# Kernel tuning notes

Hardware: AMD Instinct MI355X
Metric: run time of the kernel (lower is better)

Reference implementation:

```python
import jax, jax.numpy as jnp
import numpy as np
import math

E = 8          # num_experts (= max_expert_num)
M = 1024       # hidden_size
H = 4096       # expert FFN dim (4*hidden)
B, S = 4, 4096 # batch, seq
CAP_FACTOR = 1.0
MIN_CAPACITY = 4


def setup_inputs() -> dict:
    key = jax.random.key(0)
    ks = jax.random.split(key, 5)
    hidden_states = jax.random.normal(ks[0], (B, S, M), dtype=jnp.float32)
    wg = jax.random.normal(ks[1], (M, E), dtype=jnp.float32) * (M ** -0.5)  # gate Linear (no bias, as in TopKGate)
    w1 = jax.random.normal(ks[2], (E, M, H), dtype=jnp.float32) * (M ** -0.5)
    b1 = jnp.zeros((E, H), dtype=jnp.float32)
    w2 = jax.random.normal(ks[3], (E, H, M), dtype=jnp.float32) * (H ** -0.5)
    b2 = jnp.zeros((E, M), dtype=jnp.float32)
    return {"hidden_states": hidden_states, "wg": wg, "w1": w1, "b1": b1, "w2": w2, "b2": b2}


def reference(hidden_states, wg, w1, b1, w2, b2):
    b, s_len, m = hidden_states.shape
    x = hidden_states.reshape(-1, m)            # [s, m], s = tokens
    s = x.shape[0]
    capacity = max(int(math.ceil(s / E * CAP_FACTOR)), MIN_CAPACITY)  # static

    # ---- top-1 gating (DeepSpeed top1gating, fp32, no jitter, no RTS) ----
    logits = x.astype(jnp.float32) @ wg          # [s, e]
    gates = jax.nn.softmax(logits, axis=1)
    idx = jnp.argmax(gates, axis=1)              # chosen expert per token
    mask1 = jax.nn.one_hot(idx, E, dtype=jnp.float32)
    exp_counts = jnp.sum(mask1, axis=0).astype(jnp.int32)
    ce = jnp.mean(mask1, axis=0)                 # fraction routed per expert (pre-drop)
    me = jnp.mean(gates, axis=0)
    l_aux = jnp.sum(me * ce) * E                 # load-balancing loss

    # position of each token within its expert's queue; drop past capacity
    locations = jnp.cumsum(mask1, axis=0) - 1.0  # [s, e]
    loc = jnp.sum(locations * mask1, axis=1).astype(jnp.int32)  # [s]
    keep = (loc < capacity).astype(jnp.float32)  # capacity drop mask
    gate_s = jnp.sum(gates * mask1, axis=1) * keep
    loc_c = jnp.clip(loc, 0, capacity - 1)

    # ---- dispatch: scatter tokens to [E, C, M] slots (equiv. to einsum('sec,sm->ecm')) ----
    dispatched = jnp.zeros((E, capacity, m), dtype=x.dtype).at[idx, loc_c].add(x * keep[:, None])

    # ---- grouped expert GEMMs (MLP with GELU) ----
    h = jax.nn.gelu(jnp.einsum('ecm,emh->ech', dispatched, w1) + b1[:, None, :])
    eout = jnp.einsum('ech,ehm->ecm', h, w2) + b2[:, None, :]

    # ---- combine: gather back and scale by gate value (dropped tokens -> 0) ----
    out = eout[idx, loc_c] * gate_s[:, None]     # [s, m]
    return out.reshape(b, s_len, m), l_aux, exp_counts
```

## Files before the change

### kernel.cpp

```cpp
#include <hip/hip_runtime.h>
#include <hip/hip_bf16.h>

#define TOKENS 16384
#define MDIM   1024
#define HDIM   4096
#define NEXP   8
#define EGRP   4
#define CAP    2048
#define NKT1   (MDIM / 64)
#define NKT2   (HDIM / 64)

typedef __attribute__((ext_vector_type(8))) short bf16x8;
typedef __attribute__((ext_vector_type(4))) float f32x4;

__device__ __forceinline__ short f2bf(float x) {
  unsigned u = __float_as_uint(x);
  unsigned r = (u + 0x7fffu + ((u >> 16) & 1u)) >> 16;
  return (short)r;
}

__device__ __forceinline__ unsigned bfbits(float x) {
  unsigned u = __float_as_uint(x);
  return u + 0x7fffu + ((u >> 16) & 1u);
}

__device__ __forceinline__ float gelu_f(float x) {
  float u = 1.5957691216057308f * (x + 0.044715f * x * x * x);
  float e = __expf(u);
  return x * (1.f - 1.f / (e + 1.f));
}

__global__ __launch_bounds__(256) void gating_kernel(
    const float* __restrict__ x, const float* __restrict__ wg,
    int* __restrict__ idx, float* __restrict__ gate,
    float* __restrict__ mepart, short* __restrict__ xb) {
  __shared__ float me_s[NEXP];
  int tid = threadIdx.x, wid = tid >> 6, lane = tid & 63;
  if (tid < NEXP) me_s[tid] = 0.f;
  __syncthreads();
  int t = blockIdx.x * 4 + wid;
  float acc[NEXP];
#pragma unroll
  for (int e = 0; e < NEXP; e++) acc[e] = 0.f;
  const float4* xr = (const float4*)(x + (size_t)t * MDIM);
  short* xbr = xb + (size_t)t * MDIM + lane * 16;
#pragma unroll
  for (int j = 0; j < 4; j++) {
    float4 xv = xr[lane * 4 + j];
    short4 bv; bv.x = f2bf(xv.x); bv.y = f2bf(xv.y); bv.z = f2bf(xv.z); bv.w = f2bf(xv.w);
    ((short4*)(xbr))[j] = bv;
    int base = lane * 16 + j * 4;
    const float* xp = &xv.x;
#pragma unroll
    for (int i = 0; i < 4; i++) {
      float xi = xp[i];
      const float4* wr = (const float4*)(wg + (size_t)(base + i) * NEXP);
      float4 w0 = wr[0], w1 = wr[1];
      acc[0] += xi * w0.x; acc[1] += xi * w0.y; acc[2] += xi * w0.z; acc[3] += xi * w0.w;
      acc[4] += xi * w1.x; acc[5] += xi * w1.y; acc[6] += xi * w1.z; acc[7] += xi * w1.w;
    }
  }
#pragma unroll
  for (int off = 32; off > 0; off >>= 1)
#pragma unroll
    for (int e = 0; e < NEXP; e++) acc[e] += __shfl_xor(acc[e], off, 64);
  if (lane == 0) {
    float mx = acc[0]; int ai = 0;
#pragma unroll
    for (int e = 1; e < NEXP; e++) if (acc[e] > mx) { mx = acc[e]; ai = e; }
    float ex[NEXP]; float se = 0.f;
#pragma unroll
    for (int e = 0; e < NEXP; e++) { ex[e] = __expf(acc[e] - mx); se += ex[e]; }
    float inv = 1.f / se;
#pragma unroll
    for (int e = 0; e < NEXP; e++) atomicAdd(&me_s[e], ex[e] * inv);
    idx[t] = ai;
    gate[t] = inv;
  }
  __syncthreads();
  if (tid < NEXP) mepart[blockIdx.x * NEXP + tid] = me_s[tid];
}

__global__ __launch_bounds__(1024) void scan_kernel(
    const int* __restrict__ idx, float* __restrict__ gate,
    int* __restrict__ s2t, int* __restrict__ counts,
    const float* __restrict__ mepart, float* __restrict__ out_tail) {
  __shared__ int wcnt[16][NEXP];
  __shared__ int wbase[16][NEXP];
  __shared__ int totc[NEXP];
  __shared__ float red2[1024];
  int tid = threadIdx.x, wid = tid >> 6, lane = tid & 63;
  unsigned long long ltmask = (1ull << lane) - 1ull;
  int myexp[16], myloc[16];
  int cnt[NEXP];
#pragma unroll
  for (int e = 0; e < NEXP; e++) cnt[e] = 0;
  int base_tok = wid * 1024;
#pragma unroll
  for (int p = 0; p < 16; p++) {
    int e = idx[base_tok + p * 64 + lane];
    myexp[p] = e;
    int pos = 0;
#pragma unroll
    for (int e2 = 0; e2 < NEXP; e2++) {
      unsigned long long b = __ballot(e == e2);
      if (e == e2) pos = cnt[e2] + __popcll(b & ltmask);
      cnt[e2] += __popcll(b);
    }
    myloc[p] = pos;
  }
  if (lane < NEXP) wcnt[wid][lane] = cnt[lane];
  __syncthreads();
  if (tid < 128) {
    int w = tid >> 3, e = tid & 7;
    int s = 0;
    for (int w2 = 0; w2 < w; w2++) s += wcnt[w2][e];
    wbase[w][e] = s;
  }
  __syncthreads();
#pragma unroll
  for (int p = 0; p < 16; p++) {
    int i = base_tok + p * 64 + lane;
    int e = myexp[p];
    int loc = wbase[wid][e] + myloc[p];
    if (loc < CAP) s2t[e * CAP + loc] = i;
    else           gate[i] = 0.f;
  }
  if (tid < NEXP) {
    int tot = 0;
#pragma unroll
    for (int w = 0; w < 16; w++) tot += wcnt[w][tid];
    counts[tid] = tot;
    totc[tid] = tot;
  }
  float s = 0.f;
  int e2 = tid & 7;
  for (int r = tid >> 3; r < (TOKENS / 4); r += 128) s += mepart[(size_t)r * NEXP + e2];
  red2[tid] = s;
  __syncthreads();
#pragma unroll
  for (int off = 512; off >= 8; off >>= 1) {
    if (tid < off) red2[tid] += red2[tid + off];
    __syncthreads();
  }
  if (tid == 0) {
    float la = 0.f;
    for (int k = 0; k < NEXP; k++)
      la += (red2[k] / (float)TOKENS) * ((float)totc[k] / (float)TOKENS);
    out_tail[0] = la * (float)NEXP;
  }
  if (tid < NEXP) out_tail[1 + tid] = (float)totc[tid];
}

__global__ __launch_bounds__(256) void transpose_cvt_kernel(
    const float* __restrict__ in, short* __restrict__ out, int R, int Cc) {
  __shared__ short tile[64][72];
  int e = blockIdx.z;
  const float* in_e = in + (size_t)e * R * Cc;
  short* out_e = out + (size_t)e * R * Cc;
  int r0 = blockIdx.y * 64, c0 = blockIdx.x * 64;
  int tid = threadIdx.x;
#pragma unroll
  for (int i = 0; i < 4; i++) {
    int linear = tid + 256 * i;
    int r = linear >> 4;
    int f4 = linear & 15;
    float4 v = *(const float4*)(in_e + (size_t)(r0 + r) * Cc + c0 + f4 * 4);
    int c = f4 * 4;
    tile[c + 0][r] = f2bf(v.x);
    tile[c + 1][r] = f2bf(v.y);
    tile[c + 2][r] = f2bf(v.z);
    tile[c + 3][r] = f2bf(v.w);
  }
  __syncthreads();
#pragma unroll
  for (int i = 0; i < 4; i++) {
    int linear = tid + 256 * i;
    int c = linear >> 4;
    int s4 = linear & 15;
    short4 s;
    s.x = tile[c][s4 * 4 + 0]; s.y = tile[c][s4 * 4 + 1];
    s.z = tile[c][s4 * 4 + 2]; s.w = tile[c][s4 * 4 + 3];
    *(short4*)(out_e + (size_t)(c0 + c) * R + r0 + s4 * 4) = s;
  }
}

__device__ __forceinline__ void bar() {
  asm volatile("" ::: "memory");
  __builtin_amdgcn_s_barrier();
  asm volatile("" ::: "memory");
}
__device__ __forceinline__ void lgkm0() {
  asm volatile("s_waitcnt lgkmcnt(0)" ::: "memory");
  __builtin_amdgcn_sched_barrier(0);
}
__device__ __forceinline__ void vm_bar8() {
  asm volatile("s_waitcnt vmcnt(8)" ::: "memory");
  __builtin_amdgcn_s_barrier();
  asm volatile("" ::: "memory");
}
__device__ __forceinline__ void vm_bar6() {
  asm volatile("s_waitcnt vmcnt(6)" ::: "memory");
  __builtin_amdgcn_s_barrier();
  asm volatile("" ::: "memory");
}
__device__ __forceinline__ void vm_bar0() {
  asm volatile("s_waitcnt vmcnt(0)" ::: "memory");
  __builtin_amdgcn_s_barrier();
  asm volatile("" ::: "memory");
}

#define GLL(gp, lp) __builtin_amdgcn_global_load_lds(                                   \
    (const __attribute__((address_space(1))) void*)(gp),                                \
    (__attribute__((address_space(3))) void*)(lp), 16, 0, 0)

__global__ __launch_bounds__(512, 2) void gemm1_kernel(
    const short* __restrict__ xb, const int* __restrict__ s2t,
    const short* __restrict__ W1t, const float* __restrict__ b1,
    short* __restrict__ Hh, const short* __restrict__ zrow, int eg) {
  __shared__ __align__(16) short ldsA[2][256 * 64];
  __shared__ __align__(16) short ldsB[2][256 * 64];
  int bz = blockIdx.z, bm = blockIdx.y, bn = blockIdx.x;
  int e_abs = eg + bz;
  int tid = threadIdx.x, lane = tid & 63, w = tid >> 6;
  int v = tid >> 3;
  int sl = tid & 7;

  const short* aptr[4];
#pragma unroll
  for (int q = 0; q < 4; q++) {
    int r = q * 64 + v;
    int tok = s2t[e_abs * CAP + bm * 256 + r];
    const short* basep = (tok >= 0) ? (xb + (size_t)tok * MDIM) : zrow;
    aptr[q] = basep + ((sl ^ (r & 7)) * 8);
  }
  const short* Be = W1t + ((size_t)e_abs * HDIM + (size_t)bn * 256) * MDIM;
  const short* bptr[2][2];
#pragma unroll
  for (int h = 0; h < 2; h++)
#pragma unroll
    for (int j = 0; j < 2; j++) {
      int r = j * 128 + (v >> 5) * 64 + (v & 31) + h * 32;
      bptr[h][j] = Be + (size_t)r * MDIM + ((sl ^ (r & 7)) * 8);
    }
  asm volatile("" ::: "memory");

  int ldsa_base[4], ldsb_base[2][2];
#pragma unroll
  for (int q = 0; q < 4; q++) ldsa_base[q] = (q * 64 + w * 8) * 64;
#pragma unroll
  for (int h = 0; h < 2; h++)
#pragma unroll
    for (int j = 0; j < 2; j++)
      ldsb_base[h][j] = (j * 128 + h * 32 + (w >> 2) * 64 + (w & 3) * 8) * 64;

  GLL(aptr[0] + 0,        &ldsA[0][ldsa_base[0]]);
  GLL(aptr[2] + 0,        &ldsA[0][ldsa_base[2]]);
  GLL(bptr[0][0] + 0,     &ldsB[0][ldsb_base[0][0]]);
  GLL(bptr[0][1] + 0,     &ldsB[0][ldsb_base[0][1]]);
  GLL(bptr[1][0] + 0,     &ldsB[0][ldsb_base[1][0]]);
  GLL(bptr[1][1] + 0,     &ldsB[0][ldsb_base[1][1]]);
  GLL(aptr[1] + 0,        &ldsA[0][ldsa_base[1]]);
  GLL(aptr[3] + 0,        &ldsA[0][ldsa_base[3]]);
  GLL(aptr[0] + 64,       &ldsA[1][ldsa_base[0]]);
  GLL(aptr[2] + 64,       &ldsA[1][ldsa_base[2]]);
  GLL(bptr[0][0] + 64,    &ldsB[1][ldsb_base[0][0]]);
  GLL(bptr[0][1] + 64,    &ldsB[1][ldsb_base[0][1]]);
  GLL(bptr[1][0] + 64,    &ldsB[1][ldsb_base[1][0]]);
  GLL(bptr[1][1] + 64,    &ldsB[1][ldsb_base[1][1]]);
  GLL(aptr[1] + 64,       &ldsA[1][ldsa_base[1]]);
  GLL(aptr[3] + 64,       &ldsA[1][ldsa_base[3]]);
  vm_bar8();

  int wm = w >> 2, wn = w & 3;
  int ln = lane & 15, q4 = lane >> 4;
  int offk0 = ((q4 ^ (lane & 7)) * 8);
  int offk1 = (((4 + q4) ^ (lane & 7)) * 8);
  int arowbase = wm * 128 + ln;
  int browbase = wn * 64 + ln;

  f32x4 acc[8][4];
  f32x4 zero = {0.f, 0.f, 0.f, 0.f};
#pragma unroll
  for (int a = 0; a < 8; a++)
#pragma unroll
    for (int b = 0; b < 4; b++) acc[a][b] = zero;

  for (int t = 0; t < NKT1; ++t) {
    int cur = t & 1;
    const short* La = ldsA[cur];
    const short* Lb = ldsB[cur];
    int kts = (t + 2) * 64;
    bool st = (t + 2) < NKT1;
    bool steady = t < (NKT1 - 2);
    bf16x8 af[4][2], bf0[2][2], bf1[2][2];
#pragma unroll
    for (int rt = 0; rt < 4; rt++) {
      int ro = (arowbase + rt * 16) * 64;
      af[rt][0] = *(const bf16x8*)(La + ro + offk0);
      af[rt][1] = *(const bf16x8*)(La + ro + offk1);
    }
#pragma unroll
    for (int c = 0; c < 2; c++) {
      int ro = (browbase + c * 16) * 64;
      bf0[c][0] = *(const bf16x8*)(Lb + ro + offk0);
      bf0[c][1] = *(const bf16x8*)(Lb + ro + offk1);
    }
    bar();
    lgkm0();
    __builtin_amdgcn_s_setprio(1);
#pragma unroll
    for (int kk = 0; kk < 2; kk++)
#pragma unroll
      for (int rt = 0; rt < 4; rt++)
#pragma unroll
        for (int c = 0; c < 2; c++)
          acc[rt][c] = __builtin_amdgcn_mfma_f32_16x16x32_bf16(bf0[c][kk], af[rt][kk], acc[rt][c], 0, 0, 0);
    __builtin_amdgcn_s_setprio(0);
    bar();
    if (st) {
      GLL(aptr[0] + kts,    &ldsA[cur][ldsa_base[0]]);
      GLL(aptr[2] + kts,    &ldsA[cur][ldsa_base[2]]);
      GLL(bptr[0][0] + kts, &ldsB[cur][ldsb_base[0][0]]);
      GLL(bptr[0][1] + kts, &ldsB[cur][ldsb_base[0][1]]);
    }
#pragma unroll
    for (int c = 0; c < 2; c++) {
      int ro = (browbase + (c + 2) * 16) * 64;
      bf1[c][0] = *(const bf16x8*)(Lb + ro + offk0);
      bf1[c][1] = *(const bf16x8*)(Lb + ro + offk1);
    }
    bar();
    lgkm0();
    __builtin_amdgcn_s_setprio(1);
#pragma unroll
    for (int kk = 0; kk < 2; kk++)
#pragma unroll
      for (int rt = 0; rt < 4; rt++)
#pragma unroll
        for (int c = 0; c < 2; c++)
          acc[rt][c + 2] = __builtin_amdgcn_mfma_f32_16x16x32_bf16(bf1[c][kk], af[rt][kk], acc[rt][c + 2], 0, 0, 0);
    __builtin_amdgcn_s_setprio(0);
    bar();
    if (st) {
      GLL(bptr[1][0] + kts, &ldsB[cur][ldsb_base[1][0]]);
      GLL(bptr[1][1] + kts, &ldsB[cur][ldsb_base[1][1]]);
    }
#pragma unroll
    for (int rt = 0; rt < 4; rt++) {
      int ro = (arowbase + 64 + rt * 16) * 64;
      af[rt][0] = *(const bf16x8*)(La + ro + offk0);
      af[rt][1] = *(const bf16x8*)(La + ro + offk1);
    }
    bar();
    lgkm0();
    __builtin_amdgcn_s_setprio(1);
#pragma unroll
    for (int kk = 0; kk < 2; kk++)
#pragma unroll
      for (int rt = 0; rt < 4; rt++)
#pragma unroll
        for (int c = 0; c < 2; c++)
          acc[4 + rt][c] = __builtin_amdgcn_mfma_f32_16x16x32_bf16(bf0[c][kk], af[rt][kk], acc[4 + rt][c], 0, 0, 0);
    __builtin_amdgcn_s_setprio(0);
    bar();
    if (st) {
      GLL(aptr[1] + kts,    &ldsA[cur][ldsa_base[1]]);
      GLL(aptr[3] + kts,    &ldsA[cur][ldsa_base[3]]);
    }
    bar();
    lgkm0();
    __builtin_amdgcn_s_setprio(1);
#pragma unroll
    for (int kk = 0; kk < 2; kk++)
#pragma unroll
      for (int rt = 0; rt < 4; rt++)
#pragma unroll
        for (int c = 0; c < 2; c++)
          acc[4 + rt][c + 2] = __builtin_amdgcn_mfma_f32_16x16x32_bf16(bf1[c][kk], af[rt][kk], acc[4 + rt][c + 2], 0, 0, 0);
    __builtin_amdgcn_s_setprio(0);
    if (steady) vm_bar8(); else vm_bar0();
  }

#pragma unroll
  for (int rt = 0; rt < 8; rt++) {
    int caprow = bm * 256 + wm * 128 + rt * 16 + ln;
    size_t rowoff = ((size_t)bz * CAP + caprow) * HDIM;
#pragma unroll
    for (int c = 0; c < 4; c++) {
      int colb = bn * 256 + wn * 64 + c * 16 + q4 * 4;
      float4 bias = *(const float4*)(b1 + (size_t)e_abs * HDIM + colb);
      unsigned u0 = bfbits(gelu_f(acc[rt][c][0] + bias.x));
      unsigned u1 = bfbits(gelu_f(acc[rt][c][1] + bias.y));
      unsigned u2 = bfbits(gelu_f(acc[rt][c][2] + bias.z));
      unsigned u3 = bfbits(gelu_f(acc[rt][c][3] + bias.w));
      uint2 pk;
      pk.x = __builtin_amdgcn_perm(u1, u0, 0x07060302u);
      pk.y = __builtin_amdgcn_perm(u3, u2, 0x07060302u);
      *(uint2*)(Hh + rowoff + colb) = pk;
    }
  }
}

__global__ __launch_bounds__(512, 2) void gemm2_kernel(
    const short* __restrict__ Hh, const short* __restrict__ W2t,
    const float* __restrict__ b2, const int* __restrict__ s2t,
    const float* __restrict__ gate, float* __restrict__ out, int eg) {
  __shared__ __align__(16) short ldsA[2][128 * 64];
  __shared__ __align__(16) short ldsB[2][256 * 64];
  int bz = blockIdx.z, bm = blockIdx.y, bn = blockIdx.x;
  int e_abs = eg + bz;
  int tid = threadIdx.x, lane = tid & 63, w = tid >> 6;
  int v = tid >> 3, sl = tid & 7;
  const short* Ae = Hh + ((size_t)bz * CAP + (size_t)bm * 128) * HDIM;
  const short* Be = W2t + ((size_t)e_abs * MDIM + (size_t)bn * 256) * HDIM;
  const short* aptr[2];
#pragma unroll
  for (int h = 0; h < 2; h++) {
    int r = (v >> 5) * 64 + (v & 31) + h * 32;
    aptr[h] = Ae + (size_t)r * HDIM + ((sl ^ (r & 7)) * 8);
  }
  const short* bptr[4];
#pragma unroll
  for (int q = 0; q < 4; q++) {
    int r = q * 64 + v;
    bptr[q] = Be + (size_t)r * HDIM + ((sl ^ (r & 7)) * 8);
  }
  int ldsa_base[2], ldsb_base[4];
#pragma unroll
  for (int h = 0; h < 2; h++) ldsa_base[h] = (h * 32 + (w >> 2) * 64 + (w & 3) * 8) * 64;
#pragma unroll
  for (int q = 0; q < 4; q++) ldsb_base[q] = (q * 64 + w * 8) * 64;

  GLL(aptr[0] + 0,  &ldsA[0][ldsa_base[0]]);
  GLL(bptr[0] + 0,  &ldsB[0][ldsb_base[0]]);
  GLL(bptr[1] + 0,  &ldsB[0][ldsb_base[1]]);
  GLL(bptr[2] + 0,  &ldsB[0][ldsb_base[2]]);
  GLL(bptr[3] + 0,  &ldsB[0][ldsb_base[3]]);
  GLL(aptr[1] + 0,  &ldsA[0][ldsa_base[1]]);
  GLL(aptr[0] + 64, &ldsA[1][ldsa_base[0]]);
  GLL(bptr[0] + 64, &ldsB[1][ldsb_base[0]]);
  GLL(bptr[1] + 64, &ldsB[1][ldsb_base[1]]);
  GLL(bptr[2] + 64, &ldsB[1][ldsb_base[2]]);
  GLL(bptr[3] + 64, &ldsB[1][ldsb_base[3]]);
  asm volatile("s_waitcnt vmcnt(5)" ::: "memory");
  __builtin_amdgcn_s_barrier();
  asm volatile("" ::: "memory");

  int wm = w >> 2, wn = w & 3;
  int ln = lane & 15, q4 = lane >> 4;
  int offk0 = ((q4 ^ (lane & 7)) * 8);
  int offk1 = (((4 + q4) ^ (lane & 7)) * 8);
  int arowbase = wm * 64 + ln;
  int browbase = wn * 64 + ln;

  f32x4 acc[4][4];
  f32x4 zero = {0.f, 0.f, 0.f, 0.f};
#pragma unroll
  for (int a = 0; a < 4; a++)
#pragma unroll
    for (int b = 0; b < 4; b++) acc[a][b] = zero;

  for (int t = 0; t < NKT2; ++t) {
    int cur = t & 1;
    const short* La = ldsA[cur];
    const short* Lb = ldsB[cur];
    bool steady = t < (NKT2 - 2);
    bf16x8 af[2][2], bf[4][2];
    if (t + 1 < NKT2) { GLL(aptr[1] + (t + 1) * 64, &ldsA[cur ^ 1][ldsa_base[1]]); }
#pragma unroll
    for (int rt = 0; rt < 2; rt++) {
      int ro = (arowbase + rt * 16) * 64;
      af[rt][0] = *(const bf16x8*)(La + ro + offk0);
      af[rt][1] = *(const bf16x8*)(La + ro + offk1);
    }
#pragma unroll
    for (int c = 0; c < 4; c++) {
      int ro = (browbase + c * 16) * 64;
      bf[c][0] = *(const bf16x8*)(Lb + ro + offk0);
      bf[c][1] = *(const bf16x8*)(Lb + ro + offk1);
    }
    bar();
    lgkm0();
    __builtin_amdgcn_s_setprio(1);
#pragma unroll
    for (int kk = 0; kk < 2; kk++)
#pragma unroll
      for (int rt = 0; rt < 2; rt++)
#pragma unroll
        for (int c = 0; c < 4; c++)
          acc[rt][c] = __builtin_amdgcn_mfma_f32_16x16x32_bf16(bf[c][kk], af[rt][kk], acc[rt][c], 0, 0, 0);
    __builtin_amdgcn_s_setprio(0);
    if (steady) vm_bar6(); else vm_bar0();
    if (t + 2 < NKT2) {
      int kts = (t + 2) * 64;
      GLL(aptr[0] + kts, &ldsA[cur][ldsa_base[0]]);
      GLL(bptr[0] + kts, &ldsB[cur][ldsb_base[0]]);
      GLL(bptr[1] + kts, &ldsB[cur][ldsb_base[1]]);
      GLL(bptr[2] + kts, &ldsB[cur][ldsb_base[2]]);
      GLL(bptr[3] + kts, &ldsB[cur][ldsb_base[3]]);
    }
#pragma unroll
    for (int rt = 0; rt < 2; rt++) {
      int ro = (arowbase + 32 + rt * 16) * 64;
      af[rt][0] = *(const bf16x8*)(La + ro + offk0);
      af[rt][1] = *(const bf16x8*)(La + ro + offk1);
    }
    bar();
    lgkm0();
    __builtin_amdgcn_s_setprio(1);
#pragma unroll
    for (int kk = 0; kk < 2; kk++)
#pragma unroll
      for (int rt = 0; rt < 2; rt++)
#pragma unroll
        for (int c = 0; c < 4; c++)
          acc[2 + rt][c] = __builtin_amdgcn_mfma_f32_16x16x32_bf16(bf[c][kk], af[rt][kk], acc[2 + rt][c], 0, 0, 0);
    __builtin_amdgcn_s_setprio(0);
    if (steady) vm_bar6(); else vm_bar0();
  }

#pragma unroll
  for (int rt = 0; rt < 4; rt++) {
    int caprow = bm * 128 + wm * 64 + rt * 16 + ln;
    int token = s2t[e_abs * CAP + caprow];
    if (token < 0) continue;
    float g = gate[token];
    float* orow = out + (size_t)token * MDIM;
#pragma unroll
    for (int c = 0; c < 4; c++) {
      int colb = bn * 256 + wn * 64 + c * 16 + q4 * 4;
      float4 bias = *(const float4*)(b2 + (size_t)e_abs * MDIM + colb);
      float4 vv;
      vv.x = (acc[rt][c][0] + bias.x) * g;
      vv.y = (acc[rt][c][1] + bias.y) * g;
      vv.z = (acc[rt][c][2] + bias.z) * g;
      vv.w = (acc[rt][c][3] + bias.w) * g;
      *(float4*)(orow + colb) = vv;
    }
  }
}

__global__ __launch_bounds__(256) void zerodrop_kernel(
    const float* __restrict__ gate, float* __restrict__ out) {
  int t = blockIdx.x;
  if (gate[t] != 0.f) return;
  float4 z = {0.f, 0.f, 0.f, 0.f};
  ((float4*)(out + (size_t)t * MDIM))[threadIdx.x] = z;
}

extern "C" void kernel_launch(void* const* d_in, const int* in_sizes, int n_in,
                              void* d_out, int out_size, void* d_ws, size_t ws_size,
                              hipStream_t stream) {
  const float* x  = (const float*)d_in[0];
  const float* wg = (const float*)d_in[1];
  const float* w1 = (const float*)d_in[2];
  const float* b1 = (const float*)d_in[3];
  const float* w2 = (const float*)d_in[4];
  const float* b2 = (const float*)d_in[5];
  float* out = (float*)d_out;

  char* ws = (char*)d_ws;
  size_t off = 0;
  auto alloc = [&](size_t n) { char* ptr = ws + off; off += (n + 255) & ~(size_t)255; return ptr; };
  short* W1t  = (short*)alloc((size_t)NEXP * MDIM * HDIM * 2);
  short* W2t  = (short*)alloc((size_t)NEXP * MDIM * HDIM * 2);
  short* Hh   = (short*)alloc((size_t)EGRP * CAP * HDIM * 2);
  short* xb   = (short*)alloc((size_t)TOKENS * MDIM * 2);
  short* zrow = (short*)alloc((size_t)MDIM * 2);
  int*   idx  = (int*)  alloc(TOKENS * 4);
  float* gate = (float*)alloc(TOKENS * 4);
  int*   s2t  = (int*)  alloc(NEXP * CAP * 4);
  float* mep  = (float*)alloc((TOKENS / 4) * NEXP * 4);
  int*   cnts = (int*)  alloc(NEXP * 4);
  if (ws_size < off) return;

  hipMemsetAsync(s2t, 0xFF, NEXP * CAP * 4, stream);
  hipMemsetAsync(zrow, 0, MDIM * 2, stream);

  gating_kernel<<<TOKENS / 4, 256, 0, stream>>>(x, wg, idx, gate, mep, xb);
  scan_kernel<<<1, 1024, 0, stream>>>(idx, gate, s2t, cnts, mep, out + (size_t)TOKENS * MDIM);
  transpose_cvt_kernel<<<dim3(HDIM / 64, MDIM / 64, NEXP), 256, 0, stream>>>(w1, W1t, MDIM, HDIM);
  transpose_cvt_kernel<<<dim3(MDIM / 64, HDIM / 64, NEXP), 256, 0, stream>>>(w2, W2t, HDIM, MDIM);
  for (int g = 0; g < 2; g++) {
    gemm1_kernel<<<dim3(HDIM / 256, CAP / 256, EGRP), 512, 0, stream>>>(xb, s2t, W1t, b1, Hh, zrow, g * EGRP);
    gemm2_kernel<<<dim3(MDIM / 256, CAP / 128, EGRP), 512, 0, stream>>>(Hh, W2t, b2, s2t, gate, out, g * EGRP);
  }
  zerodrop_kernel<<<TOKENS, 256, 0, stream>>>(gate, out);
}
```

Baseline: 933.3 us.

## Restructure expert GEMM pipelines with fewer barriers, triple-buffered B, and block swizzle

Both expert GEMM kernels are reworked. Their K-loops drop the intermediate barrier/lgkm waits and issue all MFMAs for a fragment set back to back. gemm1 loads B rows contiguously and prefetches half of A one stage ahead. gemm2 triple-buffers the B tile in LDS and loads the full A tile per step. A flat-index swizzle remaps block IDs so consecutive blocks cover different M/N tiles, aiming at better cache locality. The changes cut synchronisation overhead and improve load/compute overlap, at the cost of more LDS in gemm2 and possible occupancy loss or LDS race hazards from the removed barriers.

```diff
diff --git a/kernel.cpp b/kernel.cpp
--- a/kernel.cpp
+++ b/kernel.cpp
@@ -185,22 +185,13 @@
   }
 }
 
-__device__ __forceinline__ void bar() {
-  asm volatile("" ::: "memory");
-  __builtin_amdgcn_s_barrier();
-  asm volatile("" ::: "memory");
-}
-__device__ __forceinline__ void lgkm0() {
-  asm volatile("s_waitcnt lgkmcnt(0)" ::: "memory");
-  __builtin_amdgcn_sched_barrier(0);
-}
 __device__ __forceinline__ void vm_bar8() {
   asm volatile("s_waitcnt vmcnt(8)" ::: "memory");
   __builtin_amdgcn_s_barrier();
   asm volatile("" ::: "memory");
 }
-__device__ __forceinline__ void vm_bar6() {
-  asm volatile("s_waitcnt vmcnt(6)" ::: "memory");
+__device__ __forceinline__ void vm_bar4() {
+  asm volatile("s_waitcnt vmcnt(4)" ::: "memory");
   __builtin_amdgcn_s_barrier();
   asm volatile("" ::: "memory");
 }
@@ -220,7 +211,9 @@
     short* __restrict__ Hh, const short* __restrict__ zrow, int eg) {
   __shared__ __align__(16) short ldsA[2][256 * 64];
   __shared__ __align__(16) short ldsB[2][256 * 64];
-  int bz = blockIdx.z, bm = blockIdx.y, bn = blockIdx.x;
+  int flat = blockIdx.x + 16 * blockIdx.y + 128 * blockIdx.z;
+  int swz = (flat & 7) * 64 + (flat >> 3);
+  int bn = swz & 15, bm = (swz >> 4) & 7, bz = swz >> 7;
   int e_abs = eg + bz;
   int tid = threadIdx.x, lane = tid & 63, w = tid >> 6;
   int v = tid >> 3;
@@ -235,41 +228,32 @@
     aptr[q] = basep + ((sl ^ (r & 7)) * 8);
   }
   const short* Be = W1t + ((size_t)e_abs * HDIM + (size_t)bn * 256) * MDIM;
-  const short* bptr[2][2];
-#pragma unroll
-  for (int h = 0; h < 2; h++)
-#pragma unroll
-    for (int j = 0; j < 2; j++) {
-      int r = j * 128 + (v >> 5) * 64 + (v & 31) + h * 32;
-      bptr[h][j] = Be + (size_t)r * MDIM + ((sl ^ (r & 7)) * 8);
-    }
+  const short* bptr[4];
+#pragma unroll
+  for (int q = 0; q < 4; q++) {
+    int r = q * 64 + v;
+    bptr[q] = Be + (size_t)r * MDIM + ((sl ^ (r & 7)) * 8);
+  }
   asm volatile("" ::: "memory");
 
-  int ldsa_base[4], ldsb_base[2][2];
-#pragma unroll
-  for (int q = 0; q < 4; q++) ldsa_base[q] = (q * 64 + w * 8) * 64;
-#pragma unroll
-  for (int h = 0; h < 2; h++)
-#pragma unroll
-    for (int j = 0; j < 2; j++)
-      ldsb_base[h][j] = (j * 128 + h * 32 + (w >> 2) * 64 + (w & 3) * 8) * 64;
-
-  GLL(aptr[0] + 0,        &ldsA[0][ldsa_base[0]]);
-  GLL(aptr[2] + 0,        &ldsA[0][ldsa_base[2]]);
-  GLL(bptr[0][0] + 0,     &ldsB[0][ldsb_base[0][0]]);
-  GLL(bptr[0][1] + 0,     &ldsB[0][ldsb_base[0][1]]);
-  GLL(bptr[1][0] + 0,     &ldsB[0][ldsb_base[1][0]]);
-  GLL(bptr[1][1] + 0,     &ldsB[0][ldsb_base[1][1]]);
-  GLL(aptr[1] + 0,        &ldsA[0][ldsa_base[1]]);
-  GLL(aptr[3] + 0,        &ldsA[0][ldsa_base[3]]);
-  GLL(aptr[0] + 64,       &ldsA[1][ldsa_base[0]]);
-  GLL(aptr[2] + 64,       &ldsA[1][ldsa_base[2]]);
-  GLL(bptr[0][0] + 64,    &ldsB[1][ldsb_base[0][0]]);
-  GLL(bptr[0][1] + 64,    &ldsB[1][ldsb_base[0][1]]);
-  GLL(bptr[1][0] + 64,    &ldsB[1][ldsb_base[1][0]]);
-  GLL(bptr[1][1] + 64,    &ldsB[1][ldsb_base[1][1]]);
-  GLL(aptr[1] + 64,       &ldsA[1][ldsa_base[1]]);
-  GLL(aptr[3] + 64,       &ldsA[1][ldsa_base[3]]);
+  int ldsa_base[4], ldsb_base[4];
+#pragma unroll
+  for (int q = 0; q < 4; q++) { ldsa_base[q] = (q * 64 + w * 8) * 64; ldsb_base[q] = (q * 64 + w * 8) * 64; }
+
+  GLL(aptr[0] + 0,  &ldsA[0][ldsa_base[0]]);
+  GLL(aptr[2] + 0,  &ldsA[0][ldsa_base[2]]);
+  GLL(bptr[0] + 0,  &ldsB[0][ldsb_base[0]]);
+  GLL(bptr[1] + 0,  &ldsB[0][ldsb_base[1]]);
+  GLL(bptr[2] + 0,  &ldsB[0][ldsb_base[2]]);
+  GLL(bptr[3] + 0,  &ldsB[0][ldsb_base[3]]);
+  GLL(aptr[1] + 0,  &ldsA[0][ldsa_base[1]]);
+  GLL(aptr[3] + 0,  &ldsA[0][ldsa_base[3]]);
+  GLL(aptr[0] + 64, &ldsA[1][ldsa_base[0]]);
+  GLL(aptr[2] + 64, &ldsA[1][ldsa_base[2]]);
+  GLL(bptr[0] + 64, &ldsB[1][ldsb_base[0]]);
+  GLL(bptr[1] + 64, &ldsB[1][ldsb_base[1]]);
+  GLL(bptr[2] + 64, &ldsB[1][ldsb_base[2]]);
+  GLL(bptr[3] + 64, &ldsB[1][ldsb_base[3]]);
   vm_bar8();
 
   int wm = w >> 2, wn = w & 3;
@@ -290,10 +274,13 @@
     int cur = t & 1;
     const short* La = ldsA[cur];
     const short* Lb = ldsB[cur];
-    int kts = (t + 2) * 64;
-    bool st = (t + 2) < NKT1;
     bool steady = t < (NKT1 - 2);
-    bf16x8 af[4][2], bf0[2][2], bf1[2][2];
+    bf16x8 af[4][2], bfr[4][2];
+    if (t + 1 < NKT1) {
+      int k1 = (t + 1) * 64;
+      GLL(aptr[1] + k1, &ldsA[cur ^ 1][ldsa_base[1]]);
+      GLL(aptr[3] + k1, &ldsA[cur ^ 1][ldsa_base[3]]);
+    }
 #pragma unroll
     for (int rt = 0; rt < 4; rt++) {
       int ro = (arowbase + rt * 16) * 64;
@@ -301,50 +288,29 @@
       af[rt][1] = *(const bf16x8*)(La + ro + offk1);
     }
 #pragma unroll
-    for (int c = 0; c < 2; c++) {
+    for (int c = 0; c < 4; c++) {
       int ro = (browbase + c * 16) * 64;
-      bf0[c][0] = *(const bf16x8*)(Lb + ro + offk0);
-      bf0[c][1] = *(const bf16x8*)(Lb + ro + offk1);
-    }
-    bar();
-    lgkm0();
+      bfr[c][0] = *(const bf16x8*)(Lb + ro + offk0);
+      bfr[c][1] = *(const bf16x8*)(Lb + ro + offk1);
+    }
     __builtin_amdgcn_s_setprio(1);
 #pragma unroll
-    for (int kk = 0; kk < 2; kk++)
-#pragma unroll
-      for (int rt = 0; rt < 4; rt++)
-#pragma unroll
-        for (int c = 0; c < 2; c++)
-          acc[rt][c] = __builtin_amdgcn_mfma_f32_16x16x32_bf16(bf0[c][kk], af[rt][kk], acc[rt][c], 0, 0, 0);
+    for (int rt = 0; rt < 4; rt++)
+#pragma unroll
+      for (int c = 0; c < 4; c++) {
+        acc[rt][c] = __builtin_amdgcn_mfma_f32_16x16x32_bf16(bfr[c][0], af[rt][0], acc[rt][c], 0, 0, 0);
+        acc[rt][c] = __builtin_amdgcn_mfma_f32_16x16x32_bf16(bfr[c][1], af[rt][1], acc[rt][c], 0, 0, 0);
+      }
     __builtin_amdgcn_s_setprio(0);
-    bar();
-    if (st) {
-      GLL(aptr[0] + kts,    &ldsA[cur][ldsa_base[0]]);
-      GLL(aptr[2] + kts,    &ldsA[cur][ldsa_base[2]]);
-      GLL(bptr[0][0] + kts, &ldsB[cur][ldsb_base[0][0]]);
-      GLL(bptr[0][1] + kts, &ldsB[cur][ldsb_base[0][1]]);
-    }
-#pragma unroll
-    for (int c = 0; c < 2; c++) {
-      int ro = (browbase + (c + 2) * 16) * 64;
-      bf1[c][0] = *(const bf16x8*)(Lb + ro + offk0);
-      bf1[c][1] = *(const bf16x8*)(Lb + ro + offk1);
-    }
-    bar();
-    lgkm0();
-    __builtin_amdgcn_s_setprio(1);
-#pragma unroll
-    for (int kk = 0; kk < 2; kk++)
-#pragma unroll
-      for (int rt = 0; rt < 4; rt++)
-#pragma unroll
-        for (int c = 0; c < 2; c++)
-          acc[rt][c + 2] = __builtin_amdgcn_mfma_f32_16x16x32_bf16(bf1[c][kk], af[rt][kk], acc[rt][c + 2], 0, 0, 0);
-    __builtin_amdgcn_s_setprio(0);
-    bar();
-    if (st) {
-      GLL(bptr[1][0] + kts, &ldsB[cur][ldsb_base[1][0]]);
-      GLL(bptr[1][1] + kts, &ldsB[cur][ldsb_base[1][1]]);
+    if (steady) vm_bar8(); else vm_bar0();
+    if (t + 2 < NKT1) {
+      int kts = (t + 2) * 64;
+      GLL(aptr[0] + kts, &ldsA[cur][ldsa_base[0]]);
+      GLL(aptr[2] + kts, &ldsA[cur][ldsa_base[2]]);
+      GLL(bptr[0] + kts, &ldsB[cur][ldsb_base[0]]);
+      GLL(bptr[1] + kts, &ldsB[cur][ldsb_base[1]]);
+      GLL(bptr[2] + kts, &ldsB[cur][ldsb_base[2]]);
+      GLL(bptr[3] + kts, &ldsB[cur][ldsb_base[3]]);
     }
 #pragma unroll
     for (int rt = 0; rt < 4; rt++) {
@@ -352,32 +318,14 @@
       af[rt][0] = *(const bf16x8*)(La + ro + offk0);
       af[rt][1] = *(const bf16x8*)(La + ro + offk1);
     }
-    bar();
-    lgkm0();
     __builtin_amdgcn_s_setprio(1);
 #pragma unroll
-    for (int kk = 0; kk < 2; kk++)
-#pragma unroll
-      for (int rt = 0; rt < 4; rt++)
-#pragma unroll
-        for (int c = 0; c < 2; c++)
-          acc[4 + rt][c] = __builtin_amdgcn_mfma_f32_16x16x32_bf16(bf0[c][kk], af[rt][kk], acc[4 + rt][c], 0, 0, 0);
-    __builtin_amdgcn_s_setprio(0);
-    bar();
-    if (st) {
-      GLL(aptr[1] + kts,    &ldsA[cur][ldsa_base[1]]);
-      GLL(aptr[3] + kts,    &ldsA[cur][ldsa_base[3]]);
-    }
-    bar();
-    lgkm0();
-    __builtin_amdgcn_s_setprio(1);
-#pragma unroll
-    for (int kk = 0; kk < 2; kk++)
-#pragma unroll
-      for (int rt = 0; rt < 4; rt++)
-#pragma unroll
-        for (int c = 0; c < 2; c++)
-          acc[4 + rt][c + 2] = __builtin_amdgcn_mfma_f32_16x16x32_bf16(bf1[c][kk], af[rt][kk], acc[4 + rt][c + 2], 0, 0, 0);
+    for (int rt = 0; rt < 4; rt++)
+#pragma unroll
+      for (int c = 0; c < 4; c++) {
+        acc[4 + rt][c] = __builtin_amdgcn_mfma_f32_16x16x32_bf16(bfr[c][0], af[rt][0], acc[4 + rt][c], 0, 0, 0);
+        acc[4 + rt][c] = __builtin_amdgcn_mfma_f32_16x16x32_bf16(bfr[c][1], af[rt][1], acc[4 + rt][c], 0, 0, 0);
+      }
     __builtin_amdgcn_s_setprio(0);
     if (steady) vm_bar8(); else vm_bar0();
   }
@@ -407,8 +355,10 @@
     const float* __restrict__ b2, const int* __restrict__ s2t,
     const float* __restrict__ gate, float* __restrict__ out, int eg) {
   __shared__ __align__(16) short ldsA[2][128 * 64];
-  __shared__ __align__(16) short ldsB[2][256 * 64];
-  int bz = blockIdx.z, bm = blockIdx.y, bn = blockIdx.x;
+  __shared__ __align__(16) short ldsB[3][256 * 64];
+  int flat = blockIdx.x + 4 * blockIdx.y + 64 * blockIdx.z;
+  int swz = (flat & 7) * 32 + (flat >> 3);
+  int bn = swz & 3, bm = (swz >> 2) & 15, bz = swz >> 6;
   int e_abs = eg + bz;
   int tid = threadIdx.x, lane = tid & 63, w = tid >> 6;
   int v = tid >> 3, sl = tid & 7;
@@ -417,7 +367,7 @@
   const short* aptr[2];
 #pragma unroll
   for (int h = 0; h < 2; h++) {
-    int r = (v >> 5) * 64 + (v & 31) + h * 32;
+    int r = h * 64 + v;
     aptr[h] = Ae + (size_t)r * HDIM + ((sl ^ (r & 7)) * 8);
   }
   const short* bptr[4];
@@ -428,24 +378,21 @@
   }
   int ldsa_base[2], ldsb_base[4];
 #pragma unroll
-  for (int h = 0; h < 2; h++) ldsa_base[h] = (h * 32 + (w >> 2) * 64 + (w & 3) * 8) * 64;
+  for (int h = 0; h < 2; h++) ldsa_base[h] = (h * 64 + w * 8) * 64;
 #pragma unroll
   for (int q = 0; q < 4; q++) ldsb_base[q] = (q * 64 + w * 8) * 64;
 
   GLL(aptr[0] + 0,  &ldsA[0][ldsa_base[0]]);
+  GLL(aptr[1] + 0,  &ldsA[0][ldsa_base[1]]);
   GLL(bptr[0] + 0,  &ldsB[0][ldsb_base[0]]);
   GLL(bptr[1] + 0,  &ldsB[0][ldsb_base[1]]);
   GLL(bptr[2] + 0,  &ldsB[0][ldsb_base[2]]);
   GLL(bptr[3] + 0,  &ldsB[0][ldsb_base[3]]);
-  GLL(aptr[1] + 0,  &ldsA[0][ldsa_base[1]]);
-  GLL(aptr[0] + 64, &ldsA[1][ldsa_base[0]]);
   GLL(bptr[0] + 64, &ldsB[1][ldsb_base[0]]);
   GLL(bptr[1] + 64, &ldsB[1][ldsb_base[1]]);
   GLL(bptr[2] + 64, &ldsB[1][ldsb_base[2]]);
   GLL(bptr[3] + 64, &ldsB[1][ldsb_base[3]]);
-  asm volatile("s_waitcnt vmcnt(5)" ::: "memory");
-  __builtin_amdgcn_s_barrier();
-  asm volatile("" ::: "memory");
+  vm_bar4();
 
   int wm = w >> 2, wn = w & 3;
   int ln = lane & 15, q4 = lane >> 4;
@@ -461,15 +408,29 @@
 #pragma unroll
     for (int b = 0; b < 4; b++) acc[a][b] = zero;
 
+  short* b_cur = ldsB[0];
+  short* b_n1  = ldsB[1];
+  short* b_n2  = ldsB[2];
+
   for (int t = 0; t < NKT2; ++t) {
-    int cur = t & 1;
-    const short* La = ldsA[cur];
-    const short* Lb = ldsB[cur];
+    const short* La = ldsA[t & 1];
+    const short* Lb = b_cur;
     bool steady = t < (NKT2 - 2);
-    bf16x8 af[2][2], bf[4][2];
-    if (t + 1 < NKT2) { GLL(aptr[1] + (t + 1) * 64, &ldsA[cur ^ 1][ldsa_base[1]]); }
-#pragma unroll
-    for (int rt = 0; rt < 2; rt++) {
+    if (t + 1 < NKT2) {
+      int k1 = (t + 1) * 64;
+      GLL(aptr[0] + k1, &ldsA[(t + 1) & 1][ldsa_base[0]]);
+      GLL(aptr[1] + k1, &ldsA[(t + 1) & 1][ldsa_base[1]]);
+    }
+    if (t + 2 < NKT2) {
+      int k2 = (t + 2) * 64;
+      GLL(bptr[0] + k2, b_n2 + ldsb_base[0]);
+      GLL(bptr[1] + k2, b_n2 + ldsb_base[1]);
+      GLL(bptr[2] + k2, b_n2 + ldsb_base[2]);
+      GLL(bptr[3] + k2, b_n2 + ldsb_base[3]);
+    }
+    bf16x8 af[4][2], bf[4][2];
+#pragma unroll
+    for (int rt = 0; rt < 4; rt++) {
       int ro = (arowbase + rt * 16) * 64;
       af[rt][0] = *(const bf16x8*)(La + ro + offk0);
       af[rt][1] = *(const bf16x8*)(La + ro + offk1);
@@ -480,44 +441,17 @@
       bf[c][0] = *(const bf16x8*)(Lb + ro + offk0);
       bf[c][1] = *(const bf16x8*)(Lb + ro + offk1);
     }
-    bar();
-    lgkm0();
     __builtin_amdgcn_s_setprio(1);
 #pragma unroll
-    for (int kk = 0; kk < 2; kk++)
-#pragma unroll
-      for (int rt = 0; rt < 2; rt++)
-#pragma unroll
-        for (int c = 0; c < 4; c++)
-          acc[rt][c] = __builtin_amdgcn_mfma_f32_16x16x32_bf16(bf[c][kk], af[rt][kk], acc[rt][c], 0, 0, 0);
+    for (int rt = 0; rt < 4; rt++)
+#pragma unroll
+      for (int c = 0; c < 4; c++) {
+        acc[rt][c] = __builtin_amdgcn_mfma_f32_16x16x32_bf16(bf[c][0], af[rt][0], acc[rt][c], 0, 0, 0);
+        acc[rt][c] = __builtin_amdgcn_mfma_f32_16x16x32_bf16(bf[c][1], af[rt][1], acc[rt][c], 0, 0, 0);
+      }
     __builtin_amdgcn_s_setprio(0);
-    if (steady) vm_bar6(); else vm_bar0();
-    if (t + 2 < NKT2) {
-      int kts = (t + 2) * 64;
-      GLL(aptr[0] + kts, &ldsA[cur][ldsa_base[0]]);
-      GLL(bptr[0] + kts, &ldsB[cur][ldsb_base[0]]);
-      GLL(bptr[1] + kts, &ldsB[cur][ldsb_base[1]]);
-      GLL(bptr[2] + kts, &ldsB[cur][ldsb_base[2]]);
-      GLL(bptr[3] + kts, &ldsB[cur][ldsb_base[3]]);
-    }
-#pragma unroll
-    for (int rt = 0; rt < 2; rt++) {
-      int ro = (arowbase + 32 + rt * 16) * 64;
-      af[rt][0] = *(const bf16x8*)(La + ro + offk0);
-      af[rt][1] = *(const bf16x8*)(La + ro + offk1);
-    }
-    bar();
-    lgkm0();
-    __builtin_amdgcn_s_setprio(1);
-#pragma unroll
-    for (int kk = 0; kk < 2; kk++)
-#pragma unroll
-      for (int rt = 0; rt < 2; rt++)
-#pragma unroll
-        for (int c = 0; c < 4; c++)
-          acc[2 + rt][c] = __builtin_amdgcn_mfma_f32_16x16x32_bf16(bf[c][kk], af[rt][kk], acc[2 + rt][c], 0, 0, 0);
-    __builtin_amdgcn_s_setprio(0);
-    if (steady) vm_bar6(); else vm_bar0();
+    if (steady) vm_bar4(); else vm_bar0();
+    short* tmp = b_cur; b_cur = b_n1; b_n1 = b_n2; b_n2 = tmp;
   }
 
 #pragma unroll
```

New measurement: 888.3 us. 4.8% less time.

## Swizzle GEMM block order, trim gemm1 barriers, retile gemm2 to 128x128

Applied to the files above, without the earlier changes.

Both expert GEMMs now remap their flat block index so that consecutive blocks spread across the grid, aiming for better L2 reuse of weights and activations. gemm1 drops the extra barrier and lgkmcnt waits around each MFMA phase and relies on the vmcnt barriers to order LDS reuse, which should cut synchronisation stalls. gemm2 moves from 512-thread 128x256 tiles with a two-deep staged prefetch to 256-thread 128x128 tiles with a simple one-ahead double buffer and a full vmcnt(0) barrier every K step. This doubles the gemm2 grid but may expose more global-load latency.

```diff
diff --git a/kernel.cpp b/kernel.cpp
--- a/kernel.cpp
+++ b/kernel.cpp
@@ -185,22 +185,8 @@
   }
 }
 
-__device__ __forceinline__ void bar() {
-  asm volatile("" ::: "memory");
-  __builtin_amdgcn_s_barrier();
-  asm volatile("" ::: "memory");
-}
-__device__ __forceinline__ void lgkm0() {
-  asm volatile("s_waitcnt lgkmcnt(0)" ::: "memory");
-  __builtin_amdgcn_sched_barrier(0);
-}
 __device__ __forceinline__ void vm_bar8() {
   asm volatile("s_waitcnt vmcnt(8)" ::: "memory");
-  __builtin_amdgcn_s_barrier();
-  asm volatile("" ::: "memory");
-}
-__device__ __forceinline__ void vm_bar6() {
-  asm volatile("s_waitcnt vmcnt(6)" ::: "memory");
   __builtin_amdgcn_s_barrier();
   asm volatile("" ::: "memory");
 }
@@ -220,7 +206,9 @@
     short* __restrict__ Hh, const short* __restrict__ zrow, int eg) {
   __shared__ __align__(16) short ldsA[2][256 * 64];
   __shared__ __align__(16) short ldsB[2][256 * 64];
-  int bz = blockIdx.z, bm = blockIdx.y, bn = blockIdx.x;
+  int flat = blockIdx.x + 16 * blockIdx.y + 128 * blockIdx.z;
+  int swz = (flat & 7) * 64 + (flat >> 3);
+  int bn = swz & 15, bm = (swz >> 4) & 7, bz = swz >> 7;
   int e_abs = eg + bz;
   int tid = threadIdx.x, lane = tid & 63, w = tid >> 6;
   int v = tid >> 3;
@@ -295,19 +283,17 @@
     bool steady = t < (NKT1 - 2);
     bf16x8 af[4][2], bf0[2][2], bf1[2][2];
 #pragma unroll
+    for (int c = 0; c < 2; c++) {
+      int ro = (browbase + c * 16) * 64;
+      bf0[c][0] = *(const bf16x8*)(Lb + ro + offk0);
+      bf0[c][1] = *(const bf16x8*)(Lb + ro + offk1);
+    }
+#pragma unroll
     for (int rt = 0; rt < 4; rt++) {
       int ro = (arowbase + rt * 16) * 64;
       af[rt][0] = *(const bf16x8*)(La + ro + offk0);
       af[rt][1] = *(const bf16x8*)(La + ro + offk1);
     }
-#pragma unroll
-    for (int c = 0; c < 2; c++) {
-      int ro = (browbase + c * 16) * 64;
-      bf0[c][0] = *(const bf16x8*)(Lb + ro + offk0);
-      bf0[c][1] = *(const bf16x8*)(Lb + ro + offk1);
-    }
-    bar();
-    lgkm0();
     __builtin_amdgcn_s_setprio(1);
 #pragma unroll
     for (int kk = 0; kk < 2; kk++)
@@ -317,7 +303,7 @@
         for (int c = 0; c < 2; c++)
           acc[rt][c] = __builtin_amdgcn_mfma_f32_16x16x32_bf16(bf0[c][kk], af[rt][kk], acc[rt][c], 0, 0, 0);
     __builtin_amdgcn_s_setprio(0);
-    bar();
+    if (steady) vm_bar8(); else vm_bar0();
     if (st) {
       GLL(aptr[0] + kts,    &ldsA[cur][ldsa_base[0]]);
       GLL(aptr[2] + kts,    &ldsA[cur][ldsa_base[2]]);
@@ -330,8 +316,6 @@
       bf1[c][0] = *(const bf16x8*)(Lb + ro + offk0);
       bf1[c][1] = *(const bf16x8*)(Lb + ro + offk1);
     }
-    bar();
-    lgkm0();
     __builtin_amdgcn_s_setprio(1);
 #pragma unroll
     for (int kk = 0; kk < 2; kk++)
@@ -341,7 +325,7 @@
         for (int c = 0; c < 2; c++)
           acc[rt][c + 2] = __builtin_amdgcn_mfma_f32_16x16x32_bf16(bf1[c][kk], af[rt][kk], acc[rt][c + 2], 0, 0, 0);
     __builtin_amdgcn_s_setprio(0);
-    bar();
+    if (steady) vm_bar8(); else vm_bar0();
     if (st) {
       GLL(bptr[1][0] + kts, &ldsB[cur][ldsb_base[1][0]]);
       GLL(bptr[1][1] + kts, &ldsB[cur][ldsb_base[1][1]]);
@@ -352,8 +336,6 @@
       af[rt][0] = *(const bf16x8*)(La + ro + offk0);
       af[rt][1] = *(const bf16x8*)(La + ro + offk1);
     }
-    bar();
-    lgkm0();
     __builtin_amdgcn_s_setprio(1);
 #pragma unroll
     for (int kk = 0; kk < 2; kk++)
@@ -363,13 +345,11 @@
         for (int c = 0; c < 2; c++)
           acc[4 + rt][c] = __builtin_amdgcn_mfma_f32_16x16x32_bf16(bf0[c][kk], af[rt][kk], acc[4 + rt][c], 0, 0, 0);
     __builtin_amdgcn_s_setprio(0);
-    bar();
+    if (steady) vm_bar8(); else vm_bar0();
     if (st) {
       GLL(aptr[1] + kts,    &ldsA[cur][ldsa_base[1]]);
       GLL(aptr[3] + kts,    &ldsA[cur][ldsa_base[3]]);
     }
-    bar();
-    lgkm0();
     __builtin_amdgcn_s_setprio(1);
 #pragma unroll
     for (int kk = 0; kk < 2; kk++)
@@ -402,52 +382,39 @@
   }
 }
 
-__global__ __launch_bounds__(512, 2) void gemm2_kernel(
+__global__ __launch_bounds__(256, 2) void gemm2_kernel(
     const short* __restrict__ Hh, const short* __restrict__ W2t,
     const float* __restrict__ b2, const int* __restrict__ s2t,
     const float* __restrict__ gate, float* __restrict__ out, int eg) {
   __shared__ __align__(16) short ldsA[2][128 * 64];
-  __shared__ __align__(16) short ldsB[2][256 * 64];
-  int bz = blockIdx.z, bm = blockIdx.y, bn = blockIdx.x;
+  __shared__ __align__(16) short ldsB[2][128 * 64];
+  int flat = blockIdx.x + 8 * blockIdx.y + 128 * blockIdx.z;
+  int swz = (flat & 7) * 64 + (flat >> 3);
+  int bn = swz & 7, bm = (swz >> 3) & 15, bz = swz >> 7;
   int e_abs = eg + bz;
   int tid = threadIdx.x, lane = tid & 63, w = tid >> 6;
   int v = tid >> 3, sl = tid & 7;
   const short* Ae = Hh + ((size_t)bz * CAP + (size_t)bm * 128) * HDIM;
-  const short* Be = W2t + ((size_t)e_abs * MDIM + (size_t)bn * 256) * HDIM;
-  const short* aptr[2];
-#pragma unroll
-  for (int h = 0; h < 2; h++) {
-    int r = (v >> 5) * 64 + (v & 31) + h * 32;
-    aptr[h] = Ae + (size_t)r * HDIM + ((sl ^ (r & 7)) * 8);
-  }
+  const short* Be = W2t + ((size_t)e_abs * MDIM + (size_t)bn * 128) * HDIM;
+  const short* aptr[4];
   const short* bptr[4];
 #pragma unroll
   for (int q = 0; q < 4; q++) {
-    int r = q * 64 + v;
+    int r = q * 32 + v;
+    aptr[q] = Ae + (size_t)r * HDIM + ((sl ^ (r & 7)) * 8);
     bptr[q] = Be + (size_t)r * HDIM + ((sl ^ (r & 7)) * 8);
   }
-  int ldsa_base[2], ldsb_base[4];
-#pragma unroll
-  for (int h = 0; h < 2; h++) ldsa_base[h] = (h * 32 + (w >> 2) * 64 + (w & 3) * 8) * 64;
-#pragma unroll
-  for (int q = 0; q < 4; q++) ldsb_base[q] = (q * 64 + w * 8) * 64;
-
-  GLL(aptr[0] + 0,  &ldsA[0][ldsa_base[0]]);
-  GLL(bptr[0] + 0,  &ldsB[0][ldsb_base[0]]);
-  GLL(bptr[1] + 0,  &ldsB[0][ldsb_base[1]]);
-  GLL(bptr[2] + 0,  &ldsB[0][ldsb_base[2]]);
-  GLL(bptr[3] + 0,  &ldsB[0][ldsb_base[3]]);
-  GLL(aptr[1] + 0,  &ldsA[0][ldsa_base[1]]);
-  GLL(aptr[0] + 64, &ldsA[1][ldsa_base[0]]);
-  GLL(bptr[0] + 64, &ldsB[1][ldsb_base[0]]);
-  GLL(bptr[1] + 64, &ldsB[1][ldsb_base[1]]);
-  GLL(bptr[2] + 64, &ldsB[1][ldsb_base[2]]);
-  GLL(bptr[3] + 64, &ldsB[1][ldsb_base[3]]);
-  asm volatile("s_waitcnt vmcnt(5)" ::: "memory");
-  __builtin_amdgcn_s_barrier();
-  asm volatile("" ::: "memory");
-
-  int wm = w >> 2, wn = w & 3;
+  int lds_base[4];
+#pragma unroll
+  for (int q = 0; q < 4; q++) lds_base[q] = (q * 32 + w * 8) * 64;
+
+#pragma unroll
+  for (int q = 0; q < 4; q++) GLL(aptr[q] + 0, &ldsA[0][lds_base[q]]);
+#pragma unroll
+  for (int q = 0; q < 4; q++) GLL(bptr[q] + 0, &ldsB[0][lds_base[q]]);
+  vm_bar0();
+
+  int wm = w >> 1, wn = w & 1;
   int ln = lane & 15, q4 = lane >> 4;
   int offk0 = ((q4 ^ (lane & 7)) * 8);
   int offk1 = (((4 + q4) ^ (lane & 7)) * 8);
@@ -465,59 +432,36 @@
     int cur = t & 1;
     const short* La = ldsA[cur];
     const short* Lb = ldsB[cur];
-    bool steady = t < (NKT2 - 2);
-    bf16x8 af[2][2], bf[4][2];
-    if (t + 1 < NKT2) { GLL(aptr[1] + (t + 1) * 64, &ldsA[cur ^ 1][ldsa_base[1]]); }
-#pragma unroll
-    for (int rt = 0; rt < 2; rt++) {
-      int ro = (arowbase + rt * 16) * 64;
-      af[rt][0] = *(const bf16x8*)(La + ro + offk0);
-      af[rt][1] = *(const bf16x8*)(La + ro + offk1);
-    }
+    if (t + 1 < NKT2) {
+      int k1 = (t + 1) * 64;
+#pragma unroll
+      for (int q = 0; q < 4; q++) GLL(aptr[q] + k1, &ldsA[cur ^ 1][lds_base[q]]);
+#pragma unroll
+      for (int q = 0; q < 4; q++) GLL(bptr[q] + k1, &ldsB[cur ^ 1][lds_base[q]]);
+    }
+    bf16x8 af[4][2], bf[4][2];
 #pragma unroll
     for (int c = 0; c < 4; c++) {
       int ro = (browbase + c * 16) * 64;
       bf[c][0] = *(const bf16x8*)(Lb + ro + offk0);
       bf[c][1] = *(const bf16x8*)(Lb + ro + offk1);
     }
-    bar();
-    lgkm0();
+#pragma unroll
+    for (int rt = 0; rt < 4; rt++) {
+      int ro = (arowbase + rt * 16) * 64;
+      af[rt][0] = *(const bf16x8*)(La + ro + offk0);
+      af[rt][1] = *(const bf16x8*)(La + ro + offk1);
+    }
     __builtin_amdgcn_s_setprio(1);
 #pragma unroll
     for (int kk = 0; kk < 2; kk++)
 #pragma unroll
-      for (int rt = 0; rt < 2; rt++)
+      for (int rt = 0; rt < 4; rt++)
 #pragma unroll
         for (int c = 0; c < 4; c++)
           acc[rt][c] = __builtin_amdgcn_mfma_f32_16x16x32_bf16(bf[c][kk], af[rt][kk], acc[rt][c], 0, 0, 0);
     __builtin_amdgcn_s_setprio(0);
-    if (steady) vm_bar6(); else vm_bar0();
-    if (t + 2 < NKT2) {
-      int kts = (t + 2) * 64;
-      GLL(aptr[0] + kts, &ldsA[cur][ldsa_base[0]]);
-      GLL(bptr[0] + kts, &ldsB[cur][ldsb_base[0]]);
-      GLL(bptr[1] + kts, &ldsB[cur][ldsb_base[1]]);
-      GLL(bptr[2] + kts, &ldsB[cur][ldsb_base[2]]);
-      GLL(bptr[3] + kts, &ldsB[cur][ldsb_base[3]]);
-    }
-#pragma unroll
-    for (int rt = 0; rt < 2; rt++) {
-      int ro = (arowbase + 32 + rt * 16) * 64;
-      af[rt][0] = *(const bf16x8*)(La + ro + offk0);
-      af[rt][1] = *(const bf16x8*)(La + ro + offk1);
-    }
-    bar();
-    lgkm0();
-    __builtin_amdgcn_s_setprio(1);
-#pragma unroll
-    for (int kk = 0; kk < 2; kk++)
-#pragma unroll
-      for (int rt = 0; rt < 2; rt++)
-#pragma unroll
-        for (int c = 0; c < 4; c++)
-          acc[2 + rt][c] = __builtin_amdgcn_mfma_f32_16x16x32_bf16(bf[c][kk], af[rt][kk], acc[2 + rt][c], 0, 0, 0);
-    __builtin_amdgcn_s_setprio(0);
-    if (steady) vm_bar6(); else vm_bar0();
+    vm_bar0();
   }
 
 #pragma unroll
@@ -529,7 +473,7 @@
     float* orow = out + (size_t)token * MDIM;
 #pragma unroll
     for (int c = 0; c < 4; c++) {
-      int colb = bn * 256 + wn * 64 + c * 16 + q4 * 4;
+      int colb = bn * 128 + wn * 64 + c * 16 + q4 * 4;
       float4 bias = *(const float4*)(b2 + (size_t)e_abs * MDIM + colb);
       float4 vv;
       vv.x = (acc[rt][c][0] + bias.x) * g;
@@ -584,7 +528,7 @@
   transpose_cvt_kernel<<<dim3(MDIM / 64, HDIM / 64, NEXP), 256, 0, stream>>>(w2, W2t, HDIM, MDIM);
   for (int g = 0; g < 2; g++) {
     gemm1_kernel<<<dim3(HDIM / 256, CAP / 256, EGRP), 512, 0, stream>>>(xb, s2t, W1t, b1, Hh, zrow, g * EGRP);
-    gemm2_kernel<<<dim3(MDIM / 256, CAP / 128, EGRP), 512, 0, stream>>>(Hh, W2t, b2, s2t, gate, out, g * EGRP);
+    gemm2_kernel<<<dim3(MDIM / 128, CAP / 128, EGRP), 256, 0, stream>>>(Hh, W2t, b2, s2t, gate, out, g * EGRP);
   }
   zerodrop_kernel<<<TOKENS, 256, 0, stream>>>(gate, out);
 }
```

Result: faster. 845.5 us (-9.4%).
